# Performance work log

Hardware: AMD Instinct MI355X
Metric: run time of the kernel (lower is better)

## Reference

```python
import jax, jax.numpy as jnp
import numpy as np

D = 1024; H = 16; DH = 64; L = 4; N0 = 512; N1 = 512; NF = 16; B = 4; FF = 2730
FUSION = -1; GLOBAL = -2

# static token-type masks (zorro=True path)
_tt = np.concatenate([np.zeros(N0, np.int64), np.ones(N1, np.int64), np.full(NF, FUSION, np.int64)])
_allowed = (_tt[:, None] == _tt[None, :]) | (_tt[:, None] == FUSION)
ATTN_MASK = jnp.asarray(~_allowed)  # True = masked, shape [N, N]
_rt = np.array([0, 1, FUSION, GLOBAL], np.int64)
_pool_allowed = (_rt[:, None] == _tt[None, :]) | (_rt[:, None] == GLOBAL)
POOL_MASK = jnp.asarray(~_pool_allowed)  # [4, N]


def setup_inputs() -> dict:
    key = jax.random.key(0)
    ks = jax.random.split(key, 14)
    s = 0.02
    return {
        'm0': jax.random.normal(ks[0], (B, N0, D), jnp.float32),
        'm1': jax.random.normal(ks[1], (B, N1, D), jnp.float32),
        'fusion_tokens': jax.random.normal(ks[2], (NF, D), jnp.float32),
        'return_tokens': jax.random.normal(ks[3], (4, D), jnp.float32),
        'ln_gamma': jnp.ones((L, D), jnp.float32),
        'wq': jax.random.normal(ks[4], (L, D, H * DH), jnp.float32) * s,
        'wkv': jax.random.normal(ks[5], (L, D, 2 * H * DH), jnp.float32) * s,
        'wo': jax.random.normal(ks[6], (L, H * DH, D), jnp.float32) * s,
        'ff_w1': jax.random.normal(ks[7], (L, D, 2 * FF), jnp.float32) * s,
        'ff_w2': jax.random.normal(ks[8], (L, FF, D), jnp.float32) * s,
        'pool_wq': jax.random.normal(ks[9], (D, H * DH), jnp.float32) * s,
        'pool_wkv': jax.random.normal(ks[10], (D, 2 * H * DH), jnp.float32) * s,
        'pool_wo': jax.random.normal(ks[11], (H * DH, D), jnp.float32) * s,
        'final_gamma': jnp.ones((D,), jnp.float32),
    }


def _ln(x, g):
    mu = jnp.mean(x, axis=-1, keepdims=True)
    var = jnp.mean(jnp.square(x - mu), axis=-1, keepdims=True)
    return (x - mu) * jax.lax.rsqrt(var + 1e-5) * g


def _heads(t):  # [b, n, h*d] -> [b, h, n, d]
    b, n, _ = t.shape
    return t.reshape(b, n, H, DH).transpose(0, 2, 1, 3)


def _attn(x, ctx, wq, wkv, wo, mask):
    q = _heads(x @ wq) * (DH ** -0.5)
    k, v = map(_heads, jnp.split(ctx @ wkv, 2, axis=-1))
    sim = jnp.einsum('bhid,bhjd->bhij', q, k)
    sim = jnp.where(mask, -jnp.finfo(sim.dtype).max, sim)
    attn = jax.nn.softmax(sim, axis=-1)
    out = jnp.einsum('bhij,bhjd->bhid', attn, v)
    b, h, n, d = out.shape
    return out.transpose(0, 2, 1, 3).reshape(b, n, h * d) @ wo


def _ff(x, w1, w2):
    val, gate = jnp.split(x @ w1, 2, axis=-1)
    return (jax.nn.gelu(gate, approximate=False) * val) @ w2


def reference(m0, m1, fusion_tokens, return_tokens, ln_gamma, wq, wkv, wo, ff_w1, ff_w2, pool_wq, pool_wkv, pool_wo, final_gamma):
    b = m0.shape[0]
    fus = jnp.broadcast_to(fusion_tokens[None], (b, NF, D))
    tokens = jnp.concatenate([m0, m1, fus], axis=1)  # [B, N, D]
    for l in range(L):
        h = _ln(tokens, ln_gamma[l])
        tokens = _attn(h, h, wq[l], wkv[l], wo[l], ATTN_MASK) + tokens
        h = _ln(tokens, ln_gamma[l])
        tokens = _ff(h, ff_w1[l], ff_w2[l]) + tokens
    tokens = _ln(tokens, final_gamma)
    q = jnp.broadcast_to(return_tokens[None], (b, 4, D))
    pooled = _attn(q, tokens, pool_wq, pool_wkv, pool_wo, POOL_MASK) + return_tokens[None]
    return pooled
```

## Files before the change

### kernel.cpp

```cpp
#include <hip/hip_runtime.h>
#include <stdint.h>


#define DEV __device__ __forceinline__

typedef unsigned short u16;
typedef __attribute__((ext_vector_type(8))) __bf16 bf16x8;
typedef __attribute__((ext_vector_type(4))) float floatx4;

DEV u16 f2bf(float f) {
  union { float f; unsigned u; } v; v.f = f;
  return (u16)((v.u + 0x7fffu + ((v.u >> 16) & 1u)) >> 16);
}
DEV float bf2f(u16 s) {
  union { unsigned u; float f; } v; v.u = ((unsigned)s) << 16;
  return v.f;
}

#define MFMA(a, b, c) __builtin_amdgcn_mfma_f32_16x16x32_bf16(a, b, c, 0, 0, 0)

DEV void gld16(const u16* g, u16* l) {
  __builtin_amdgcn_global_load_lds((__attribute__((address_space(1))) void*)g,
                                   (__attribute__((address_space(3))) void*)l,
                                   16, 0, 0);
}

#define MREAL 4160
#define MPAD  4224
#define NPAD  1056
#define FFP   2816
#define FF2P  5632

__global__ __launch_bounds__(256) void transpose_cvt(
    const float* __restrict__ in, u16* __restrict__ out,
    int Kin, int N, int Kstride) {
  __shared__ float tile[32][33];
  const int k0 = blockIdx.x * 32, n0 = blockIdx.y * 32;
  const int tx = threadIdx.x, ty = threadIdx.y;
#pragma unroll
  for (int i = 0; i < 4; i++) {
    int k = k0 + ty + i * 8;
    tile[ty + i * 8][tx] = (k < Kin) ? in[(int64_t)k * N + n0 + tx] : 0.f;
  }
  __syncthreads();
#pragma unroll
  for (int i = 0; i < 4; i++) {
    int n = n0 + ty + i * 8;
    int k = k0 + tx;
    if (k < Kstride) out[(int64_t)n * Kstride + k] = f2bf(tile[tx][ty + i * 8]);
  }
}

__global__ __launch_bounds__(256) void transpose_w1(
    const float* __restrict__ in, u16* __restrict__ out) {
  __shared__ float tile[32][33];
  const int k0 = blockIdx.x * 32;
  const int r0 = blockIdx.y * 32;
  const int tx = threadIdx.x, ty = threadIdx.y;
  const int vb = (r0 >> 5) << 4;
  const int vi = vb + (tx & 15);
  const int c = (tx < 16) ? vi : 2730 + vi;
  const bool valid = vi < 2730;
#pragma unroll
  for (int i = 0; i < 4; i++) {
    int k = k0 + ty + i * 8;
    tile[ty + i * 8][tx] = valid ? in[(int64_t)k * 5460 + c] : 0.f;
  }
  __syncthreads();
#pragma unroll
  for (int i = 0; i < 4; i++) {
    int rl = ty + i * 8;
    out[(int64_t)(r0 + rl) * 1024 + k0 + tx] = f2bf(tile[tx][rl]);
  }
}

__global__ __launch_bounds__(256) void build_tokens_k(
    const float* __restrict__ m0p, const float* __restrict__ m1p,
    const float* __restrict__ fus, float* __restrict__ tokens) {
  const int n = blockIdx.x, b = blockIdx.y, t = threadIdx.x;
  const float* src = (n < 512) ? m0p + ((int64_t)b * 512 + n) * 1024
                   : (n < 1024) ? m1p + ((int64_t)b * 512 + (n - 512)) * 1024
                                : fus + (int64_t)(n - 1024) * 1024;
  float4 v = ((const float4*)src)[t];
  ((float4*)(tokens + ((int64_t)b * 1040 + n) * 1024))[t] = v;
}

__global__ __launch_bounds__(256) void ln_k(const float* __restrict__ x,
                                            const float* __restrict__ gamma,
                                            u16* __restrict__ out) {
  const int r = blockIdx.x, t = threadIdx.x;
  const float4 v = ((const float4*)(x + (int64_t)r * 1024))[t];
  float s = v.x + v.y + v.z + v.w;
  float q = v.x * v.x + v.y * v.y + v.z * v.z + v.w * v.w;
#pragma unroll
  for (int off = 32; off >= 1; off >>= 1) {
    s += __shfl_xor(s, off);
    q += __shfl_xor(q, off);
  }
  __shared__ float red[8];
  const int w = t >> 6, l = t & 63;
  if (l == 0) { red[w] = s; red[4 + w] = q; }
  __syncthreads();
  s = red[0] + red[1] + red[2] + red[3];
  q = red[4] + red[5] + red[6] + red[7];
  const float mu = s * (1.f / 1024.f);
  const float var = q * (1.f / 1024.f) - mu * mu;
  const float rs = rsqrtf(var + 1e-5f);
  const float4 g = ((const float4*)gamma)[t];
  u16* op = out + (int64_t)r * 1024 + t * 4;
  op[0] = f2bf((v.x - mu) * rs * g.x);
  op[1] = f2bf((v.y - mu) * rs * g.y);
  op[2] = f2bf((v.z - mu) * rs * g.z);
  op[3] = f2bf((v.w - mu) * rs * g.w);
}

enum { EPI_QKV = 0, EPI_KV = 1, EPI_TOKADD = 2, EPI_GG = 3 };

template <int EPI>
__global__ __launch_bounds__(256) void gemm_bt(
    const u16* __restrict__ A, const u16* __restrict__ Bt,
    int Kstr, int Mreal,
    float* __restrict__ tokens, u16* __restrict__ oq, u16* __restrict__ ok,
    u16* __restrict__ ovT, u16* __restrict__ oh2) {
  __shared__ __align__(16) u16 lA0[128 * 32];
  __shared__ __align__(16) u16 lA1[128 * 32];
  __shared__ __align__(16) u16 lB0[128 * 32];
  __shared__ __align__(16) u16 lB1[128 * 32];
  const int t = threadIdx.x;
  const int w = t >> 6, l = t & 63;
  const int lane16 = l & 15, quad = l >> 4;
  const int m0 = blockIdx.y * 128, n0 = blockIdx.x * 128;
  const int wm = (w >> 1) * 64, wn = (w & 1) * 64;

  const int Klen = Kstr / gridDim.z;
  const int koff = blockIdx.z * Klen;

  const floatx4 fz = {0.f, 0.f, 0.f, 0.f};
  floatx4 acc[4][4];
#pragma unroll
  for (int i = 0; i < 4; i++)
#pragma unroll
    for (int j = 0; j < 4; j++) acc[i][j] = fz;

  const int rowL = t >> 2;
  const int colL = (t & 3) * 8;
  const u16* gA = A + (int64_t)(m0 + rowL) * Kstr + koff + colL;
  const u16* gB = Bt + (int64_t)(n0 + rowL) * Kstr + koff + colL;
  u16* lA0p = lA0 + t * 8;
  u16* lA1p = lA1 + t * 8;
  u16* lB0p = lB0 + t * 8;
  u16* lB1p = lB1 + t * 8;
  const int fo = (wm + lane16) * 32 + quad * 8;
  const int fon = (wn + lane16) * 32 + quad * 8;
  const int64_t rsk = (int64_t)64 * Kstr;

  for (int kt = 0; kt < Klen; kt += 64) {
    gld16(gA + kt, lA0p);
    gld16(gA + kt + rsk, lA0p + 64 * 32);
    gld16(gA + kt + 32, lA1p);
    gld16(gA + kt + 32 + rsk, lA1p + 64 * 32);
    gld16(gB + kt, lB0p);
    gld16(gB + kt + rsk, lB0p + 64 * 32);
    gld16(gB + kt + 32, lB1p);
    gld16(gB + kt + 32 + rsk, lB1p + 64 * 32);
    __syncthreads();
    bf16x8 af[4], bf[4];
#pragma unroll
    for (int i = 0; i < 4; i++) af[i] = *(const bf16x8*)(lA0 + fo + i * 16 * 32);
#pragma unroll
    for (int j = 0; j < 4; j++) bf[j] = *(const bf16x8*)(lB0 + fon + j * 16 * 32);
#pragma unroll
    for (int i = 0; i < 4; i++)
#pragma unroll
      for (int j = 0; j < 4; j++) acc[i][j] = MFMA(af[i], bf[j], acc[i][j]);
#pragma unroll
    for (int i = 0; i < 4; i++) af[i] = *(const bf16x8*)(lA1 + fo + i * 16 * 32);
#pragma unroll
    for (int j = 0; j < 4; j++) bf[j] = *(const bf16x8*)(lB1 + fon + j * 16 * 32);
#pragma unroll
    for (int i = 0; i < 4; i++)
#pragma unroll
      for (int j = 0; j < 4; j++) acc[i][j] = MFMA(af[i], bf[j], acc[i][j]);
    __syncthreads();
  }

  if constexpr (EPI == EPI_TOKADD) {
    const bool atomic = gridDim.z > 1;
#pragma unroll
    for (int i = 0; i < 4; i++) {
      const int mb = m0 + wm + i * 16 + quad * 4;
#pragma unroll
      for (int reg = 0; reg < 4; reg++) {
        const int m = mb + reg;
        if (m < Mreal) {
          float* tp = tokens + (int64_t)m * 1024;
#pragma unroll
          for (int j = 0; j < 4; j++) {
            const int n = n0 + wn + j * 16 + lane16;
            if (atomic) atomicAdd(tp + n, acc[i][j][reg]);
            else tp[n] += acc[i][j][reg];
          }
        }
      }
    }
  } else if constexpr (EPI == EPI_QKV) {
#pragma unroll
    for (int i = 0; i < 4; i++) {
      const int mb = m0 + wm + i * 16 + quad * 4;
#pragma unroll
      for (int reg = 0; reg < 4; reg++) {
        const int m = mb + reg;
        if (m < Mreal) {
          const int b = m / 1040, rb = m % 1040;
#pragma unroll
          for (int j = 0; j < 4; j++) {
            const int n = n0 + wn + j * 16 + lane16;
            const float v = acc[i][j][reg];
            if (n < 1024) {
              const int hd = n >> 6, d = n & 63;
              oq[(((int64_t)b * 16 + hd) * NPAD + rb) * 64 + d] = f2bf(v * 0.125f);
            } else if (n < 2048) {
              const int n2 = n - 1024;
              const int hd = n2 >> 6, d = n2 & 63;
              ok[(((int64_t)b * 16 + hd) * NPAD + rb) * 64 + d] = f2bf(v);
            } else {
              const int n2 = n - 2048;
              const int hd = n2 >> 6, d = n2 & 63;
              ovT[(((int64_t)b * 16 + hd) * 64 + d) * NPAD + rb] = f2bf(v);
            }
          }
        }
      }
    }
  } else if constexpr (EPI == EPI_KV) {
#pragma unroll
    for (int i = 0; i < 4; i++) {
      const int mb = m0 + wm + i * 16 + quad * 4;
#pragma unroll
      for (int reg = 0; reg < 4; reg++) {
        const int m = mb + reg;
        if (m < Mreal) {
          const int b = m / 1040, rb = m % 1040;
#pragma unroll
          for (int j = 0; j < 4; j++) {
            const int n = n0 + wn + j * 16 + lane16;
            const float v = acc[i][j][reg];
            if (n < 1024) {
              const int hd = n >> 6, d = n & 63;
              ok[(((int64_t)b * 16 + hd) * NPAD + rb) * 64 + d] = f2bf(v);
            } else {
              const int n2 = n - 1024;
              const int hd = n2 >> 6, d = n2 & 63;
              ovT[(((int64_t)b * 16 + hd) * 64 + d) * NPAD + rb] = f2bf(v);
            }
          }
        }
      }
    }
  } else {
#pragma unroll
    for (int i = 0; i < 4; i++) {
      const int mb = m0 + wm + i * 16 + quad * 4;
#pragma unroll
      for (int reg = 0; reg < 4; reg++) {
        const int m = mb + reg;
        u16* hp = oh2 + (int64_t)m * FFP;
#pragma unroll
        for (int j = 0; j < 4; j += 2) {
          const float val = acc[i][j][reg];
          const float g = acc[i][j + 1][reg];
          const float ge = 0.5f * g * (1.f + erff(g * 0.70710678118654752f));
          const int vi = (((n0 + wn + j * 16) >> 5) << 4) + lane16;
          hp[vi] = f2bf(val * ge);
        }
      }
    }
  }
}

__global__ __launch_bounds__(256) void attn_k(const u16* __restrict__ qb,
                                              const u16* __restrict__ kb,
                                              const u16* __restrict__ vTb,
                                              u16* __restrict__ ao) {
  const int t = threadIdx.x, w = t >> 6, l = t & 63;
  const int lane16 = l & 15, quad = l >> 4;
  const int bh = blockIdx.y, b = bh >> 4, h = bh & 15;
  const int row0 = blockIdx.x * 64 + w * 16;
  __shared__ __align__(16) u16 lp[4][16 * 32];
  if (row0 >= 1040) return;
  u16* myp = lp[w];
  const int type = (row0 < 512) ? 0 : (row0 < 1024 ? 1 : 2);
  const int cbeg = (type == 1) ? 512 : 0;
  const int cend = (type == 0) ? 512 : (type == 1 ? 1024 : 1040);
  const int niter = (cend - cbeg + 31) >> 5;

  const u16* qp = qb + ((int64_t)bh * NPAD + row0 + lane16) * 64 + quad * 8;
  const bf16x8 a0 = *(const bf16x8*)qp;
  const bf16x8 a1 = *(const bf16x8*)(qp + 32);

  const floatx4 fz = {0.f, 0.f, 0.f, 0.f};
  floatx4 O[4] = {fz, fz, fz, fz};
  float mrow[4] = {-1e30f, -1e30f, -1e30f, -1e30f};
  float lrow[4] = {0.f, 0.f, 0.f, 0.f};

  for (int it = 0; it < niter; ++it) {
    const int c0 = cbeg + it * 32;
    const u16* kp = kb + ((int64_t)bh * NPAD + c0 + lane16) * 64 + quad * 8;
    bf16x8 b00 = *(const bf16x8*)kp;
    bf16x8 b01 = *(const bf16x8*)(kp + 32);
    bf16x8 b10 = *(const bf16x8*)(kp + 16 * 64);
    bf16x8 b11 = *(const bf16x8*)(kp + 16 * 64 + 32);
    floatx4 s0 = MFMA(a0, b00, fz); s0 = MFMA(a1, b01, s0);
    floatx4 s1 = MFMA(a0, b10, fz); s1 = MFMA(a1, b11, s1);
    if (c0 + 32 > cend) {
      if (c0 + lane16 >= cend) { s0[0] = s0[1] = s0[2] = s0[3] = -1e30f; }
      if (c0 + 16 + lane16 >= cend) { s1[0] = s1[1] = s1[2] = s1[3] = -1e30f; }
    }
    float al[4];
#pragma unroll
    for (int r = 0; r < 4; r++) {
      float tm = fmaxf(s0[r], s1[r]);
      tm = fmaxf(tm, __shfl_xor(tm, 1));
      tm = fmaxf(tm, __shfl_xor(tm, 2));
      tm = fmaxf(tm, __shfl_xor(tm, 4));
      tm = fmaxf(tm, __shfl_xor(tm, 8));
      const float mn = fmaxf(mrow[r], tm);
      const float p0 = __expf(s0[r] - mn);
      const float p1 = __expf(s1[r] - mn);
      float ps = p0 + p1;
      ps += __shfl_xor(ps, 1); ps += __shfl_xor(ps, 2);
      ps += __shfl_xor(ps, 4); ps += __shfl_xor(ps, 8);
      const float a_ = __expf(mrow[r] - mn);
      lrow[r] = lrow[r] * a_ + ps;
      mrow[r] = mn;
      al[r] = a_;
      myp[(quad * 4 + r) * 32 + lane16] = f2bf(p0);
      myp[(quad * 4 + r) * 32 + 16 + lane16] = f2bf(p1);
    }
#pragma unroll
    for (int dt = 0; dt < 4; dt++) {
      O[dt][0] *= al[0]; O[dt][1] *= al[1];
      O[dt][2] *= al[2]; O[dt][3] *= al[3];
    }
    const bf16x8 pf = *(const bf16x8*)(myp + lane16 * 32 + quad * 8);
#pragma unroll
    for (int dt = 0; dt < 4; dt++) {
      const u16* vp = vTb + ((int64_t)bh * 64 + dt * 16 + lane16) * NPAD + c0 + quad * 8;
      const bf16x8 bv = *(const bf16x8*)vp;
      O[dt] = MFMA(pf, bv, O[dt]);
    }
  }
#pragma unroll
  for (int dt = 0; dt < 4; dt++)
#pragma unroll
    for (int r = 0; r < 4; r++) {
      const int row = row0 + quad * 4 + r;
      ao[((int64_t)b * 1040 + row) * 1024 + h * 64 + dt * 16 + lane16] =
          f2bf(O[dt][r] / lrow[r]);
    }
}

__global__ __launch_bounds__(256) void poolq_k(const float* __restrict__ rtk,
                                               const float* __restrict__ pwq,
                                               u16* __restrict__ qP) {
  const int r = blockIdx.y;
  const int n = blockIdx.x * 256 + threadIdx.x;
  const float* x = rtk + (int64_t)r * 1024;
  float acc = 0.f;
#pragma unroll 8
  for (int k = 0; k < 1024; k++) acc += x[k] * pwq[(int64_t)k * 1024 + n];
  qP[(int64_t)r * 1024 + n] = f2bf(acc * 0.125f);
}

DEV bool pvalid(int r, int c) {
  if (r == 0) return c < 512;
  if (r == 1) return (c >= 512) && (c < 1024);
  if (r == 2) return (c >= 1024) && (c < 1040);
  return c < 1040;
}

__global__ __launch_bounds__(64) void pool_attn_k(const u16* __restrict__ qP,
                                                  const u16* __restrict__ kb,
                                                  const u16* __restrict__ vTb,
                                                  u16* __restrict__ po) {
  const int l = threadIdx.x;
  const int lane16 = l & 15, quad = l >> 4;
  const int bh = blockIdx.x, b = bh >> 4, h = bh & 15;
  __shared__ __align__(16) u16 myp[16 * 32];
  const u16* qp = qP + (int64_t)lane16 * 1024 + h * 64 + quad * 8;
  const bf16x8 a0 = *(const bf16x8*)qp;
  const bf16x8 a1 = *(const bf16x8*)(qp + 32);
  const floatx4 fz = {0.f, 0.f, 0.f, 0.f};
  floatx4 O[4] = {fz, fz, fz, fz};
  float mrow[4] = {-1e30f, -1e30f, -1e30f, -1e30f};
  float lrow[4] = {0.f, 0.f, 0.f, 0.f};
  for (int it = 0; it < 33; ++it) {
    const int c0 = it * 32;
    const u16* kp = kb + ((int64_t)bh * NPAD + c0 + lane16) * 64 + quad * 8;
    bf16x8 b00 = *(const bf16x8*)kp;
    bf16x8 b01 = *(const bf16x8*)(kp + 32);
    bf16x8 b10 = *(const bf16x8*)(kp + 16 * 64);
    bf16x8 b11 = *(const bf16x8*)(kp + 16 * 64 + 32);
    floatx4 s0 = MFMA(a0, b00, fz); s0 = MFMA(a1, b01, s0);
    floatx4 s1 = MFMA(a0, b10, fz); s1 = MFMA(a1, b11, s1);
#pragma unroll
    for (int r = 0; r < 4; r++) {
      if (!pvalid(quad * 4 + r, c0 + lane16)) s0[r] = -1e30f;
      if (!pvalid(quad * 4 + r, c0 + 16 + lane16)) s1[r] = -1e30f;
    }
    float al[4];
#pragma unroll
    for (int r = 0; r < 4; r++) {
      float tm = fmaxf(s0[r], s1[r]);
      tm = fmaxf(tm, __shfl_xor(tm, 1));
      tm = fmaxf(tm, __shfl_xor(tm, 2));
      tm = fmaxf(tm, __shfl_xor(tm, 4));
      tm = fmaxf(tm, __shfl_xor(tm, 8));
      const float mn = fmaxf(mrow[r], tm);
      const float p0 = __expf(s0[r] - mn);
      const float p1 = __expf(s1[r] - mn);
      float ps = p0 + p1;
      ps += __shfl_xor(ps, 1); ps += __shfl_xor(ps, 2);
      ps += __shfl_xor(ps, 4); ps += __shfl_xor(ps, 8);
      const float a_ = __expf(mrow[r] - mn);
      lrow[r] = lrow[r] * a_ + ps;
      mrow[r] = mn;
      al[r] = a_;
      myp[(quad * 4 + r) * 32 + lane16] = f2bf(p0);
      myp[(quad * 4 + r) * 32 + 16 + lane16] = f2bf(p1);
    }
#pragma unroll
    for (int dt = 0; dt < 4; dt++) {
      O[dt][0] *= al[0]; O[dt][1] *= al[1];
      O[dt][2] *= al[2]; O[dt][3] *= al[3];
    }
    const bf16x8 pf = *(const bf16x8*)(myp + lane16 * 32 + quad * 8);
#pragma unroll
    for (int dt = 0; dt < 4; dt++) {
      const u16* vp = vTb + ((int64_t)bh * 64 + dt * 16 + lane16) * NPAD + c0 + quad * 8;
      const bf16x8 bv = *(const bf16x8*)vp;
      O[dt] = MFMA(pf, bv, O[dt]);
    }
  }
  if (quad == 0) {
#pragma unroll
    for (int dt = 0; dt < 4; dt++)
#pragma unroll
      for (int r = 0; r < 4; r++)
        po[((int64_t)b * 4 + r) * 1024 + h * 64 + dt * 16 + lane16] =
            f2bf(O[dt][r] / lrow[r]);
  }
}

__global__ __launch_bounds__(256) void fout_k(const u16* __restrict__ po,
                                              const float* __restrict__ pwo,
                                              const float* __restrict__ rtk,
                                              float* __restrict__ out) {
  const int row = blockIdx.y;
  const int n = blockIdx.x * 256 + threadIdx.x;
  const u16* x = po + (int64_t)row * 1024;
  float acc = 0.f;
#pragma unroll 8
  for (int k = 0; k < 1024; k++) acc += bf2f(x[k]) * pwo[(int64_t)k * 1024 + n];
  out[(int64_t)row * 1024 + n] = acc + rtk[(int64_t)(row & 3) * 1024 + n];
}

extern "C" void kernel_launch(void* const* d_in, const int* in_sizes, int n_in,
                              void* d_out, int out_size, void* d_ws, size_t ws_size,
                              hipStream_t stream) {
  (void)in_sizes; (void)n_in; (void)out_size; (void)ws_size;
  const float* m0p  = (const float*)d_in[0];
  const float* m1p  = (const float*)d_in[1];
  const float* fus  = (const float*)d_in[2];
  const float* rtk  = (const float*)d_in[3];
  const float* lng  = (const float*)d_in[4];
  const float* wq   = (const float*)d_in[5];
  const float* wkv  = (const float*)d_in[6];
  const float* wo   = (const float*)d_in[7];
  const float* w1   = (const float*)d_in[8];
  const float* w2   = (const float*)d_in[9];
  const float* pwq  = (const float*)d_in[10];
  const float* pwkv = (const float*)d_in[11];
  const float* pwo  = (const float*)d_in[12];
  const float* fg   = (const float*)d_in[13];
  float* out = (float*)d_out;

  char* p = (char*)d_ws;
  auto alloc = [&](size_t bytes) -> char* {
    char* r = p;
    p += (bytes + 255) & ~(size_t)255;
    return r;
  };
  u16* warena = (u16*)alloc((size_t)FF2P * 1024 * 2);
  float* tokens = (float*)alloc((size_t)MREAL * 1024 * 4);
  u16* hbuf  = (u16*)alloc((size_t)MPAD * 1024 * 2);
  u16* qb    = (u16*)alloc((size_t)64 * NPAD * 64 * 2);
  u16* kbuf  = (u16*)alloc((size_t)64 * NPAD * 64 * 2);
  u16* vTbuf = (u16*)alloc((size_t)64 * NPAD * 64 * 2);
  u16* h2buf = qb;
  u16* qP    = (u16*)alloc((size_t)16 * 1024 * 2);
  u16* poolO = (u16*)alloc((size_t)16 * 1024 * 2);

  const dim3 tb(32, 8, 1);
  build_tokens_k<<<dim3(1040, 4), 256, 0, stream>>>(m0p, m1p, fus, tokens);

  for (int lyr = 0; lyr < 4; ++lyr) {
    ln_k<<<MREAL, 256, 0, stream>>>(tokens, lng + lyr * 1024, hbuf);
    transpose_cvt<<<dim3(32, 32), tb, 0, stream>>>(
        wq + (int64_t)lyr * 1024 * 1024, warena, 1024, 1024, 1024);
    transpose_cvt<<<dim3(32, 64), tb, 0, stream>>>(
        wkv + (int64_t)lyr * 1024 * 2048, warena + (size_t)1024 * 1024, 1024, 2048, 1024);
    gemm_bt<EPI_QKV><<<dim3(24, 33), 256, 0, stream>>>(
        hbuf, warena, 1024, MREAL, nullptr, qb, kbuf, vTbuf, nullptr);
    attn_k<<<dim3(17, 64), 256, 0, stream>>>(qb, kbuf, vTbuf, hbuf);
    transpose_cvt<<<dim3(32, 32), tb, 0, stream>>>(
        wo + (int64_t)lyr * 1024 * 1024, warena, 1024, 1024, 1024);
    gemm_bt<EPI_TOKADD><<<dim3(8, 33, 2), 256, 0, stream>>>(
        hbuf, warena, 1024, MREAL, tokens, nullptr, nullptr, nullptr, nullptr);
    ln_k<<<MREAL, 256, 0, stream>>>(tokens, lng + lyr * 1024, hbuf);
    transpose_w1<<<dim3(32, FF2P / 32), tb, 0, stream>>>(
        w1 + (int64_t)lyr * 1024 * 5460, warena);
    gemm_bt<EPI_GG><<<dim3(FF2P / 128, 33), 256, 0, stream>>>(
        hbuf, warena, 1024, MREAL, nullptr, nullptr, nullptr, nullptr, h2buf);
    transpose_cvt<<<dim3(FFP / 32, 32), tb, 0, stream>>>(
        w2 + (int64_t)lyr * 2730 * 1024, warena, 2730, 1024, FFP);
    gemm_bt<EPI_TOKADD><<<dim3(8, 33, 2), 256, 0, stream>>>(
        h2buf, warena, FFP, MREAL, tokens, nullptr, nullptr, nullptr, nullptr);
  }

  ln_k<<<MREAL, 256, 0, stream>>>(tokens, fg, hbuf);
  transpose_cvt<<<dim3(32, 64), tb, 0, stream>>>(pwkv, warena, 1024, 2048, 1024);
  gemm_bt<EPI_KV><<<dim3(16, 33), 256, 0, stream>>>(
      hbuf, warena, 1024, MREAL, nullptr, nullptr, kbuf, vTbuf, nullptr);
  poolq_k<<<dim3(4, 4), 256, 0, stream>>>(rtk, pwq, qP);
  pool_attn_k<<<64, 64, 0, stream>>>(qP, kbuf, vTbuf, poolO);
  fout_k<<<dim3(4, 16), 256, 0, stream>>>(poolO, pwo, rtk, out);
}
```

Measured before the change: 1.880 ms.

## Compute transposed scores in attention to keep P in registers and skip LDS

The attention kernels now compute S^T by swapping the MFMA operands. Each lane then holds the scores of one query row across four keys, so the bf16 P fragment can be packed directly in registers for the PV MFMA without an LDS round trip. To match that register layout, the V^T store in the QKV/KV epilogues permutes key indices within each 32-block. Row max and sum reductions drop to two cross-quad shuffles, and the rescale of O is skipped when no row max changes. The pool query kernel now zero-fills 16 query rows so the unused MFMA rows are defined. This adds a coupling between the epilogue permutation and the attention fragment layout.

```diff
diff --git a/kernel.cpp b/kernel.cpp
--- a/kernel.cpp
+++ b/kernel.cpp
@@ -23,6 +23,10 @@
   __builtin_amdgcn_global_load_lds((__attribute__((address_space(1))) void*)g,
                                    (__attribute__((address_space(3))) void*)l,
                                    16, 0, 0);
+}
+
+DEV int vperm32(int j) {
+  return (((j >> 2) & 3) << 3) | (j & 3) | (((j >> 4) & 1) << 2);
 }
 
 #define MREAL 4160
@@ -212,6 +216,7 @@
         const int m = mb + reg;
         if (m < Mreal) {
           const int b = m / 1040, rb = m % 1040;
+          const int rbp = (rb & ~31) | vperm32(rb & 31);
 #pragma unroll
           for (int j = 0; j < 4; j++) {
             const int n = n0 + wn + j * 16 + lane16;
@@ -226,7 +231,7 @@
             } else {
               const int n2 = n - 2048;
               const int hd = n2 >> 6, d = n2 & 63;
-              ovT[(((int64_t)b * 16 + hd) * 64 + d) * NPAD + rb] = f2bf(v);
+              ovT[(((int64_t)b * 16 + hd) * 64 + d) * NPAD + rbp] = f2bf(v);
             }
           }
         }
@@ -241,6 +246,7 @@
         const int m = mb + reg;
         if (m < Mreal) {
           const int b = m / 1040, rb = m % 1040;
+          const int rbp = (rb & ~31) | vperm32(rb & 31);
 #pragma unroll
           for (int j = 0; j < 4; j++) {
             const int n = n0 + wn + j * 16 + lane16;
@@ -251,7 +257,7 @@
             } else {
               const int n2 = n - 1024;
               const int hd = n2 >> 6, d = n2 & 63;
-              ovT[(((int64_t)b * 16 + hd) * 64 + d) * NPAD + rb] = f2bf(v);
+              ovT[(((int64_t)b * 16 + hd) * 64 + d) * NPAD + rbp] = f2bf(v);
             }
           }
         }
@@ -284,11 +290,10 @@
                                               u16* __restrict__ ao) {
   const int t = threadIdx.x, w = t >> 6, l = t & 63;
   const int lane16 = l & 15, quad = l >> 4;
+  const int kvb = quad * 4;
   const int bh = blockIdx.y, b = bh >> 4, h = bh & 15;
   const int row0 = blockIdx.x * 64 + w * 16;
-  __shared__ __align__(16) u16 lp[4][16 * 32];
   if (row0 >= 1040) return;
-  u16* myp = lp[w];
   const int type = (row0 < 512) ? 0 : (row0 < 1024 ? 1 : 2);
   const int cbeg = (type == 1) ? 512 : 0;
   const int cend = (type == 0) ? 512 : (type == 1 ? 1024 : 1040);
@@ -297,66 +302,79 @@
   const u16* qp = qb + ((int64_t)bh * NPAD + row0 + lane16) * 64 + quad * 8;
   const bf16x8 a0 = *(const bf16x8*)qp;
   const bf16x8 a1 = *(const bf16x8*)(qp + 32);
+  const u16* vbase = vTb + ((int64_t)bh * 64 + lane16) * NPAD + quad * 8;
 
   const floatx4 fz = {0.f, 0.f, 0.f, 0.f};
   floatx4 O[4] = {fz, fz, fz, fz};
-  float mrow[4] = {-1e30f, -1e30f, -1e30f, -1e30f};
-  float lrow[4] = {0.f, 0.f, 0.f, 0.f};
+  float mrow = -1e30f, lrow = 0.f;
 
   for (int it = 0; it < niter; ++it) {
     const int c0 = cbeg + it * 32;
     const u16* kp = kb + ((int64_t)bh * NPAD + c0 + lane16) * 64 + quad * 8;
-    bf16x8 b00 = *(const bf16x8*)kp;
-    bf16x8 b01 = *(const bf16x8*)(kp + 32);
-    bf16x8 b10 = *(const bf16x8*)(kp + 16 * 64);
-    bf16x8 b11 = *(const bf16x8*)(kp + 16 * 64 + 32);
-    floatx4 s0 = MFMA(a0, b00, fz); s0 = MFMA(a1, b01, s0);
-    floatx4 s1 = MFMA(a0, b10, fz); s1 = MFMA(a1, b11, s1);
+    const bf16x8 b00 = *(const bf16x8*)kp;
+    const bf16x8 b01 = *(const bf16x8*)(kp + 32);
+    const bf16x8 b10 = *(const bf16x8*)(kp + 16 * 64);
+    const bf16x8 b11 = *(const bf16x8*)(kp + 16 * 64 + 32);
+    floatx4 s0 = MFMA(b00, a0, fz); s0 = MFMA(b01, a1, s0);
+    floatx4 s1 = MFMA(b10, a0, fz); s1 = MFMA(b11, a1, s1);
     if (c0 + 32 > cend) {
-      if (c0 + lane16 >= cend) { s0[0] = s0[1] = s0[2] = s0[3] = -1e30f; }
-      if (c0 + 16 + lane16 >= cend) { s1[0] = s1[1] = s1[2] = s1[3] = -1e30f; }
-    }
-    float al[4];
+#pragma unroll
+      for (int r = 0; r < 4; r++) {
+        if (c0 + kvb + r >= cend) s0[r] = -1e30f;
+        if (c0 + 16 + kvb + r >= cend) s1[r] = -1e30f;
+      }
+    }
+    float tm = fmaxf(fmaxf(fmaxf(s0[0], s0[1]), fmaxf(s0[2], s0[3])),
+                     fmaxf(fmaxf(s1[0], s1[1]), fmaxf(s1[2], s1[3])));
+    tm = fmaxf(tm, __shfl_xor(tm, 16));
+    tm = fmaxf(tm, __shfl_xor(tm, 32));
+    if (!__all(tm <= mrow)) {
+      const float mn = fmaxf(mrow, tm);
+      const float a_ = __expf(mrow - mn);
+      mrow = mn;
+      lrow *= a_;
+      const float al0 = __shfl(a_, kvb + 0, 16);
+      const float al1 = __shfl(a_, kvb + 1, 16);
+      const float al2 = __shfl(a_, kvb + 2, 16);
+      const float al3 = __shfl(a_, kvb + 3, 16);
+#pragma unroll
+      for (int dt = 0; dt < 4; dt++) {
+        O[dt][0] *= al0; O[dt][1] *= al1; O[dt][2] *= al2; O[dt][3] *= al3;
+      }
+    }
+    float p0[4], p1[4];
 #pragma unroll
     for (int r = 0; r < 4; r++) {
-      float tm = fmaxf(s0[r], s1[r]);
-      tm = fmaxf(tm, __shfl_xor(tm, 1));
-      tm = fmaxf(tm, __shfl_xor(tm, 2));
-      tm = fmaxf(tm, __shfl_xor(tm, 4));
-      tm = fmaxf(tm, __shfl_xor(tm, 8));
-      const float mn = fmaxf(mrow[r], tm);
-      const float p0 = __expf(s0[r] - mn);
-      const float p1 = __expf(s1[r] - mn);
-      float ps = p0 + p1;
-      ps += __shfl_xor(ps, 1); ps += __shfl_xor(ps, 2);
-      ps += __shfl_xor(ps, 4); ps += __shfl_xor(ps, 8);
-      const float a_ = __expf(mrow[r] - mn);
-      lrow[r] = lrow[r] * a_ + ps;
-      mrow[r] = mn;
-      al[r] = a_;
-      myp[(quad * 4 + r) * 32 + lane16] = f2bf(p0);
-      myp[(quad * 4 + r) * 32 + 16 + lane16] = f2bf(p1);
+      p0[r] = __expf(s0[r] - mrow);
+      p1[r] = __expf(s1[r] - mrow);
+    }
+    float ps = ((p0[0] + p0[1]) + (p0[2] + p0[3])) +
+               ((p1[0] + p1[1]) + (p1[2] + p1[3]));
+    ps += __shfl_xor(ps, 16);
+    ps += __shfl_xor(ps, 32);
+    lrow += ps;
+    union { bf16x8 v; u16 s[8]; } pf;
+#pragma unroll
+    for (int r = 0; r < 4; r++) {
+      pf.s[r] = f2bf(p0[r]);
+      pf.s[4 + r] = f2bf(p1[r]);
     }
 #pragma unroll
     for (int dt = 0; dt < 4; dt++) {
-      O[dt][0] *= al[0]; O[dt][1] *= al[1];
-      O[dt][2] *= al[2]; O[dt][3] *= al[3];
-    }
-    const bf16x8 pf = *(const bf16x8*)(myp + lane16 * 32 + quad * 8);
-#pragma unroll
-    for (int dt = 0; dt < 4; dt++) {
-      const u16* vp = vTb + ((int64_t)bh * 64 + dt * 16 + lane16) * NPAD + c0 + quad * 8;
-      const bf16x8 bv = *(const bf16x8*)vp;
-      O[dt] = MFMA(pf, bv, O[dt]);
-    }
-  }
+      const bf16x8 bv = *(const bf16x8*)(vbase + (int64_t)dt * 16 * NPAD + c0);
+      O[dt] = MFMA(pf.v, bv, O[dt]);
+    }
+  }
+  float lr[4];
+#pragma unroll
+  for (int r = 0; r < 4; r++) lr[r] = __shfl(lrow, kvb + r, 16);
 #pragma unroll
   for (int dt = 0; dt < 4; dt++)
 #pragma unroll
     for (int r = 0; r < 4; r++) {
-      const int row = row0 + quad * 4 + r;
+      const int row = row0 + kvb + r;
       ao[((int64_t)b * 1040 + row) * 1024 + h * 64 + dt * 16 + lane16] =
-          f2bf(O[dt][r] / lrow[r]);
+          f2bf(O[dt][r] / lr[r]);
     }
 }
 
@@ -365,6 +383,7 @@
                                                u16* __restrict__ qP) {
   const int r = blockIdx.y;
   const int n = blockIdx.x * 256 + threadIdx.x;
+  if (r >= 4) { qP[(int64_t)r * 1024 + n] = 0; return; }
   const float* x = rtk + (int64_t)r * 1024;
   float acc = 0.f;
 #pragma unroll 8
@@ -385,70 +404,80 @@
                                                   u16* __restrict__ po) {
   const int l = threadIdx.x;
   const int lane16 = l & 15, quad = l >> 4;
+  const int kvb = quad * 4;
   const int bh = blockIdx.x, b = bh >> 4, h = bh & 15;
-  __shared__ __align__(16) u16 myp[16 * 32];
   const u16* qp = qP + (int64_t)lane16 * 1024 + h * 64 + quad * 8;
   const bf16x8 a0 = *(const bf16x8*)qp;
   const bf16x8 a1 = *(const bf16x8*)(qp + 32);
+  const u16* vbase = vTb + ((int64_t)bh * 64 + lane16) * NPAD + quad * 8;
   const floatx4 fz = {0.f, 0.f, 0.f, 0.f};
   floatx4 O[4] = {fz, fz, fz, fz};
-  float mrow[4] = {-1e30f, -1e30f, -1e30f, -1e30f};
-  float lrow[4] = {0.f, 0.f, 0.f, 0.f};
+  float mrow = -1e30f, lrow = 0.f;
   for (int it = 0; it < 33; ++it) {
     const int c0 = it * 32;
     const u16* kp = kb + ((int64_t)bh * NPAD + c0 + lane16) * 64 + quad * 8;
-    bf16x8 b00 = *(const bf16x8*)kp;
-    bf16x8 b01 = *(const bf16x8*)(kp + 32);
-    bf16x8 b10 = *(const bf16x8*)(kp + 16 * 64);
-    bf16x8 b11 = *(const bf16x8*)(kp + 16 * 64 + 32);
-    floatx4 s0 = MFMA(a0, b00, fz); s0 = MFMA(a1, b01, s0);
-    floatx4 s1 = MFMA(a0, b10, fz); s1 = MFMA(a1, b11, s1);
+    const bf16x8 b00 = *(const bf16x8*)kp;
+    const bf16x8 b01 = *(const bf16x8*)(kp + 32);
+    const bf16x8 b10 = *(const bf16x8*)(kp + 16 * 64);
+    const bf16x8 b11 = *(const bf16x8*)(kp + 16 * 64 + 32);
+    floatx4 s0 = MFMA(b00, a0, fz); s0 = MFMA(b01, a1, s0);
+    floatx4 s1 = MFMA(b10, a0, fz); s1 = MFMA(b11, a1, s1);
 #pragma unroll
     for (int r = 0; r < 4; r++) {
-      if (!pvalid(quad * 4 + r, c0 + lane16)) s0[r] = -1e30f;
-      if (!pvalid(quad * 4 + r, c0 + 16 + lane16)) s1[r] = -1e30f;
-    }
-    float al[4];
+      if (!pvalid(lane16, c0 + kvb + r)) s0[r] = -1e30f;
+      if (!pvalid(lane16, c0 + 16 + kvb + r)) s1[r] = -1e30f;
+    }
+    float tm = fmaxf(fmaxf(fmaxf(s0[0], s0[1]), fmaxf(s0[2], s0[3])),
+                     fmaxf(fmaxf(s1[0], s1[1]), fmaxf(s1[2], s1[3])));
+    tm = fmaxf(tm, __shfl_xor(tm, 16));
+    tm = fmaxf(tm, __shfl_xor(tm, 32));
+    if (!__all(tm <= mrow)) {
+      const float mn = fmaxf(mrow, tm);
+      const float a_ = __expf(mrow - mn);
+      mrow = mn;
+      lrow *= a_;
+      const float al0 = __shfl(a_, kvb + 0, 16);
+      const float al1 = __shfl(a_, kvb + 1, 16);
+      const float al2 = __shfl(a_, kvb + 2, 16);
+      const float al3 = __shfl(a_, kvb + 3, 16);
+#pragma unroll
+      for (int dt = 0; dt < 4; dt++) {
+        O[dt][0] *= al0; O[dt][1] *= al1; O[dt][2] *= al2; O[dt][3] *= al3;
+      }
+    }
+    float p0[4], p1[4];
 #pragma unroll
     for (int r = 0; r < 4; r++) {
-      float tm = fmaxf(s0[r], s1[r]);
-      tm = fmaxf(tm, __shfl_xor(tm, 1));
-      tm = fmaxf(tm, __shfl_xor(tm, 2));
-      tm = fmaxf(tm, __shfl_xor(tm, 4));
-      tm = fmaxf(tm, __shfl_xor(tm, 8));
-      const float mn = fmaxf(mrow[r], tm);
-      const float p0 = __expf(s0[r] - mn);
-      const float p1 = __expf(s1[r] - mn);
-      float ps = p0 + p1;
-      ps += __shfl_xor(ps, 1); ps += __shfl_xor(ps, 2);
-      ps += __shfl_xor(ps, 4); ps += __shfl_xor(ps, 8);
-      const float a_ = __expf(mrow[r] - mn);
-      lrow[r] = lrow[r] * a_ + ps;
-      mrow[r] = mn;
-      al[r] = a_;
-      myp[(quad * 4 + r) * 32 + lane16] = f2bf(p0);
-      myp[(quad * 4 + r) * 32 + 16 + lane16] = f2bf(p1);
+      p0[r] = __expf(s0[r] - mrow);
+      p1[r] = __expf(s1[r] - mrow);
+    }
+    float ps = ((p0[0] + p0[1]) + (p0[2] + p0[3])) +
+               ((p1[0] + p1[1]) + (p1[2] + p1[3]));
+    ps += __shfl_xor(ps, 16);
+    ps += __shfl_xor(ps, 32);
+    lrow += ps;
+    union { bf16x8 v; u16 s[8]; } pf;
+#pragma unroll
+    for (int r = 0; r < 4; r++) {
+      pf.s[r] = f2bf(p0[r]);
+      pf.s[4 + r] = f2bf(p1[r]);
     }
 #pragma unroll
     for (int dt = 0; dt < 4; dt++) {
-      O[dt][0] *= al[0]; O[dt][1] *= al[1];
-      O[dt][2] *= al[2]; O[dt][3] *= al[3];
-    }
-    const bf16x8 pf = *(const bf16x8*)(myp + lane16 * 32 + quad * 8);
-#pragma unroll
-    for (int dt = 0; dt < 4; dt++) {
-      const u16* vp = vTb + ((int64_t)bh * 64 + dt * 16 + lane16) * NPAD + c0 + quad * 8;
-      const bf16x8 bv = *(const bf16x8*)vp;
-      O[dt] = MFMA(pf, bv, O[dt]);
-    }
-  }
+      const bf16x8 bv = *(const bf16x8*)(vbase + (int64_t)dt * 16 * NPAD + c0);
+      O[dt] = MFMA(pf.v, bv, O[dt]);
+    }
+  }
+  float lr[4];
+#pragma unroll
+  for (int r = 0; r < 4; r++) lr[r] = __shfl(lrow, r, 16);
   if (quad == 0) {
 #pragma unroll
     for (int dt = 0; dt < 4; dt++)
 #pragma unroll
       for (int r = 0; r < 4; r++)
         po[((int64_t)b * 4 + r) * 1024 + h * 64 + dt * 16 + lane16] =
-            f2bf(O[dt][r] / lrow[r]);
+            f2bf(O[dt][r] / lr[r]);
   }
 }
 
@@ -532,7 +561,7 @@
   transpose_cvt<<<dim3(32, 64), tb, 0, stream>>>(pwkv, warena, 1024, 2048, 1024);
   gemm_bt<EPI_KV><<<dim3(16, 33), 256, 0, stream>>>(
       hbuf, warena, 1024, MREAL, nullptr, nullptr, kbuf, vTbuf, nullptr);
-  poolq_k<<<dim3(4, 4), 256, 0, stream>>>(rtk, pwq, qP);
+  poolq_k<<<dim3(4, 16), 256, 0, stream>>>(rtk, pwq, qP);
   pool_attn_k<<<64, 64, 0, stream>>>(qP, kbuf, vTbuf, poolO);
   fout_k<<<dim3(4, 16), 256, 0, stream>>>(poolO, pwo, rtk, out);
 }
```

Result: no change. 1.859 ms (-1.1%).
